# Kernel tuning notes

Measured on AMD Instinct MI355X. Metric: run time of the kernel, lower is better.

## Reference

```python
import jax, jax.numpy as jnp
import numpy as np

MAX_LEN = 8192  # static bound on per-row nonzeros (jit-friendly stand-in for data-dependent max_len)
B, D, E = 256, 65536, 128
DENSITY = 0.08  # expected nnz/row ~5243 << MAX_LEN


def setup_inputs() -> dict:
    key = jax.random.key(0)
    k1, k2, k3 = jax.random.split(key, 3)
    mask = jax.random.uniform(k1, (B, D)) < DENSITY
    x = jnp.where(mask, jax.random.normal(k2, (B, D), dtype=jnp.float32), 0.0)
    embed_table = jax.random.normal(k3, (D + 1, E), dtype=jnp.float32) * 0.02
    t = jnp.zeros((1,), dtype=jnp.float32)
    return {"t": t, "x": x, "embed_table": embed_table}


def reference(t, x, embed_table):
    # --- condense: per-row stream compaction of nonzero entries ---
    d = x.shape[1]
    mask = x != 0
    idx = jnp.arange(d)
    # push positions of zero entries to the end, keep nonzero positions sorted ascending
    keys = jnp.where(mask, idx, d)              # (B, D)
    order = jnp.sort(keys, axis=1)[:, :MAX_LEN]  # (B, MAX_LEN) compacted nonzero positions (pad = d)
    valid = order < d
    p = jnp.where(valid, order + 1, 0)           # 1-based positions, 0 = pad (matches torch code)
    v = jnp.where(valid, jnp.take_along_axis(x, jnp.minimum(order, d - 1), axis=1), 0.0)
    # --- embedding lookup on condensed positions (computed as in original; unused by output) ---
    id_embed = embed_table[p]                    # (B, MAX_LEN, E)
    # --- decondense: scatter values back to dense layout ---
    rows = jnp.arange(x.shape[0])[:, None]
    tgt = jnp.where(p > 0, p - 1, 0)
    y = jnp.zeros_like(x).at[rows, tgt].add(jnp.where(p > 0, v, 0.0))
    return y
```

## Files before the change

### kernel.cpp

```cpp
#include <hip/hip_runtime.h>

#define NROWS    256
#define DCOLS    65536
#define MAXLEN   8192
#define BLKROW   8
#define K1TPB    256
#define K1V4     8
#define K2TPB    1024
#define K2V4     16
#define NWAVE2   (K2TPB / 64)


__global__ __launch_bounds__(K1TPB) void copy_count_kernel(
        const float* __restrict__ x, float* __restrict__ y,
        int* __restrict__ blk_cnt) {
    const int t    = threadIdx.x;
    const int lane = t & 63;
    const int wave = t >> 6;
    const size_t base4 = (size_t)blockIdx.x * (K1TPB * K1V4);

    const float4* __restrict__ x4 = reinterpret_cast<const float4*>(x) + base4;
    float4* __restrict__ y4       = reinterpret_cast<float4*>(y) + base4;

    int cnt = 0;
#pragma unroll
    for (int i = 0; i < K1V4; ++i) {
        float4 v = x4[i * K1TPB + t];
        cnt += (v.x != 0.0f) + (v.y != 0.0f) + (v.z != 0.0f) + (v.w != 0.0f);
        y4[i * K1TPB + t] = v;
    }

#pragma unroll
    for (int off = 32; off; off >>= 1) cnt += __shfl_xor(cnt, off, 64);

    __shared__ int wsum[K1TPB / 64];
    if (lane == 0) wsum[wave] = cnt;
    __syncthreads();
    if (t == 0) {
        int acc = 0;
#pragma unroll
        for (int w = 0; w < K1TPB / 64; ++w) acc += wsum[w];
        blk_cnt[blockIdx.x] = acc;
    }
}

__global__ __launch_bounds__(K2TPB) void fixup_kernel(
        const float* __restrict__ x, float* __restrict__ y,
        const int* __restrict__ blk_cnt) {
    const int row  = blockIdx.x;
    const int t    = threadIdx.x;
    const int lane = t & 63;
    const int wave = t >> 6;

    __shared__ int csh[BLKROW];
    if (t < BLKROW) csh[t] = blk_cnt[row * BLKROW + t];
    __syncthreads();
    int nnz = 0;
#pragma unroll
    for (int b = 0; b < BLKROW; ++b) nnz += csh[b];

    if (nnz <= MAXLEN) return;

    const float4* __restrict__ xc =
        reinterpret_cast<const float4*>(x + (size_t)row * DCOLS) + t * K2V4;
    float4* __restrict__ yc =
        reinterpret_cast<float4*>(y + (size_t)row * DCOLS) + t * K2V4;

    int ccnt = 0;
#pragma unroll
    for (int i = 0; i < K2V4; ++i) {
        float4 w = xc[i];
        ccnt += (w.x != 0.0f) + (w.y != 0.0f) + (w.z != 0.0f) + (w.w != 0.0f);
    }
    int incl = ccnt;
#pragma unroll
    for (int off = 1; off < 64; off <<= 1) {
        int n = __shfl_up(incl, off, 64);
        if (lane >= off) incl += n;
    }
    __shared__ int wsum[NWAVE2];
    __shared__ int wbase[NWAVE2];
    if (lane == 63) wsum[wave] = incl;
    __syncthreads();
    if (t == 0) {
        int acc = 0;
#pragma unroll
        for (int w = 0; w < NWAVE2; ++w) { wbase[w] = acc; acc += wsum[w]; }
    }
    __syncthreads();
    int rank = wbase[wave] + (incl - ccnt);

#pragma unroll
    for (int i = 0; i < K2V4; ++i) {
        float4 w = xc[i];
        float4 o;
        bool nx = (w.x != 0.0f); o.x = (nx && rank < MAXLEN) ? w.x : 0.0f; rank += nx;
        bool ny = (w.y != 0.0f); o.y = (ny && rank < MAXLEN) ? w.y : 0.0f; rank += ny;
        bool nz = (w.z != 0.0f); o.z = (nz && rank < MAXLEN) ? w.z : 0.0f; rank += nz;
        bool nw = (w.w != 0.0f); o.w = (nw && rank < MAXLEN) ? w.w : 0.0f; rank += nw;
        yc[i] = o;
    }
}

extern "C" void kernel_launch(void* const* d_in, const int* in_sizes, int n_in,
                              void* d_out, int out_size, void* d_ws, size_t ws_size,
                              hipStream_t stream) {
    const float* x = (const float*)d_in[1];
    float* y = (float*)d_out;
    int* blk_cnt = (int*)d_ws;

    copy_count_kernel<<<NROWS * BLKROW, K1TPB, 0, stream>>>(x, y, blk_cnt);
    fixup_kernel<<<NROWS, K2TPB, 0, stream>>>(x, y, blk_cnt);
}
```

Baseline: 138.1 us.

## Fuse count and fixup kernels via per-row atomic ticket, use nontemporal copies

Result: slower. 312.9 us (+126.6%).

```diff
diff --git a/kernel.cpp b/kernel.cpp
--- a/kernel.cpp
+++ b/kernel.cpp
@@ -4,71 +4,67 @@
 #define DCOLS    65536
 #define MAXLEN   8192
 #define BLKROW   8
-#define K1TPB    256
-#define K1V4     8
-#define K2TPB    1024
-#define K2V4     16
-#define NWAVE2   (K2TPB / 64)
+#define TPB      256
+#define V4       8
+#define NWAVE    (TPB / 64)
+#define SLOWV4   (DCOLS / 4 / TPB)
 
+typedef float f32x4 __attribute__((ext_vector_type(4)));
 
-__global__ __launch_bounds__(K1TPB) void copy_count_kernel(
+__global__ __launch_bounds__(TPB) void fused_copy_count_fix_kernel(
         const float* __restrict__ x, float* __restrict__ y,
-        int* __restrict__ blk_cnt) {
+        int* __restrict__ row_nnz, int* __restrict__ row_tkt) {
     const int t    = threadIdx.x;
     const int lane = t & 63;
     const int wave = t >> 6;
-    const size_t base4 = (size_t)blockIdx.x * (K1TPB * K1V4);
+    const int row  = blockIdx.x >> 3;
+    const size_t base4 = (size_t)blockIdx.x * (TPB * V4);
 
-    const float4* __restrict__ x4 = reinterpret_cast<const float4*>(x) + base4;
-    float4* __restrict__ y4       = reinterpret_cast<float4*>(y) + base4;
+    const f32x4* __restrict__ x4 = reinterpret_cast<const f32x4*>(x) + base4;
+    f32x4* __restrict__ y4       = reinterpret_cast<f32x4*>(y) + base4;
 
     int cnt = 0;
 #pragma unroll
-    for (int i = 0; i < K1V4; ++i) {
-        float4 v = x4[i * K1TPB + t];
+    for (int i = 0; i < V4; ++i) {
+        f32x4 v = __builtin_nontemporal_load(&x4[i * TPB + t]);
         cnt += (v.x != 0.0f) + (v.y != 0.0f) + (v.z != 0.0f) + (v.w != 0.0f);
-        y4[i * K1TPB + t] = v;
+        __builtin_nontemporal_store(v, &y4[i * TPB + t]);
     }
 
 #pragma unroll
     for (int off = 32; off; off >>= 1) cnt += __shfl_xor(cnt, off, 64);
 
-    __shared__ int wsum[K1TPB / 64];
+    __shared__ int wsum[NWAVE];
+    __shared__ int wbase[NWAVE];
+    __shared__ int sh_fix;
     if (lane == 0) wsum[wave] = cnt;
     __syncthreads();
+
     if (t == 0) {
-        int acc = 0;
+        int tot = 0;
 #pragma unroll
-        for (int w = 0; w < K1TPB / 64; ++w) acc += wsum[w];
-        blk_cnt[blockIdx.x] = acc;
+        for (int w = 0; w < NWAVE; ++w) tot += wsum[w];
+        __threadfence();
+        atomicAdd(&row_nnz[row], tot);
+        __threadfence();
+        int tk = atomicAdd(&row_tkt[row], 1);
+        int f = 0;
+        if (tk == BLKROW - 1) {
+            int nnz = atomicAdd(&row_nnz[row], 0);
+            if (nnz > MAXLEN) f = 1;
+        }
+        sh_fix = f;
     }
-}
-
-__global__ __launch_bounds__(K2TPB) void fixup_kernel(
-        const float* __restrict__ x, float* __restrict__ y,
-        const int* __restrict__ blk_cnt) {
-    const int row  = blockIdx.x;
-    const int t    = threadIdx.x;
-    const int lane = t & 63;
-    const int wave = t >> 6;
-
-    __shared__ int csh[BLKROW];
-    if (t < BLKROW) csh[t] = blk_cnt[row * BLKROW + t];
     __syncthreads();
-    int nnz = 0;
-#pragma unroll
-    for (int b = 0; b < BLKROW; ++b) nnz += csh[b];
-
-    if (nnz <= MAXLEN) return;
+    if (!sh_fix) return;
 
     const float4* __restrict__ xc =
-        reinterpret_cast<const float4*>(x + (size_t)row * DCOLS) + t * K2V4;
+        reinterpret_cast<const float4*>(x + (size_t)row * DCOLS) + t * SLOWV4;
     float4* __restrict__ yc =
-        reinterpret_cast<float4*>(y + (size_t)row * DCOLS) + t * K2V4;
+        reinterpret_cast<float4*>(y + (size_t)row * DCOLS) + t * SLOWV4;
 
     int ccnt = 0;
-#pragma unroll
-    for (int i = 0; i < K2V4; ++i) {
+    for (int i = 0; i < SLOWV4; ++i) {
         float4 w = xc[i];
         ccnt += (w.x != 0.0f) + (w.y != 0.0f) + (w.z != 0.0f) + (w.w != 0.0f);
     }
@@ -78,20 +74,17 @@
         int n = __shfl_up(incl, off, 64);
         if (lane >= off) incl += n;
     }
-    __shared__ int wsum[NWAVE2];
-    __shared__ int wbase[NWAVE2];
     if (lane == 63) wsum[wave] = incl;
     __syncthreads();
     if (t == 0) {
         int acc = 0;
 #pragma unroll
-        for (int w = 0; w < NWAVE2; ++w) { wbase[w] = acc; acc += wsum[w]; }
+        for (int w = 0; w < NWAVE; ++w) { wbase[w] = acc; acc += wsum[w]; }
     }
     __syncthreads();
     int rank = wbase[wave] + (incl - ccnt);
 
-#pragma unroll
-    for (int i = 0; i < K2V4; ++i) {
+    for (int i = 0; i < SLOWV4; ++i) {
         float4 w = xc[i];
         float4 o;
         bool nx = (w.x != 0.0f); o.x = (nx && rank < MAXLEN) ? w.x : 0.0f; rank += nx;
@@ -107,8 +100,9 @@
                               hipStream_t stream) {
     const float* x = (const float*)d_in[1];
     float* y = (float*)d_out;
-    int* blk_cnt = (int*)d_ws;
+    int* row_nnz = (int*)d_ws;
+    int* row_tkt = (int*)d_ws + NROWS;
 
-    copy_count_kernel<<<NROWS * BLKROW, K1TPB, 0, stream>>>(x, y, blk_cnt);
-    fixup_kernel<<<NROWS, K2TPB, 0, stream>>>(x, y, blk_cnt);
+    (void)hipMemsetAsync(d_ws, 0, NROWS * 2 * sizeof(int), stream);
+    fused_copy_count_fix_kernel<<<NROWS * BLKROW, TPB, 0, stream>>>(x, y, row_nnz, row_tkt);
 }
```
